# Performance work log

Hardware: AMD Instinct MI355X
Metric: run time of the kernel (lower is better)

## Reference

```python
import jax, jax.numpy as jnp
import numpy as np
import math

B, T, D = 2, 2048, 1024
NH, DH = 16, 64
MLP = 4096


def setup_inputs() -> dict:
    key = jax.random.key(0)
    ks = jax.random.split(key, 10)
    xavier = lambda k, shape: jax.random.uniform(
        k, shape, jnp.float32,
        -math.sqrt(6.0 / (shape[0] + shape[1])), math.sqrt(6.0 / (shape[0] + shape[1])))
    return {
        "inputs": jax.random.normal(ks[0], (B, T, D), jnp.float32),
        "cond": jax.random.normal(ks[1], (B, D), jnp.float32),
        "attention_mask": jnp.zeros((T, T), jnp.bool_),
        # LayerNorm params
        "ln1_g": jnp.ones((D,), jnp.float32), "ln1_b": jnp.zeros((D,), jnp.float32),
        "ln2_g": jnp.ones((D,), jnp.float32), "ln2_b": jnp.zeros((D,), jnp.float32),
        # Attention params (torch Linear stores weight as [out,in]; we store [in,out])
        "w_qkv": xavier(ks[2], (D, 3 * D)),
        "w_out": xavier(ks[3], (D, D)),
        "b_out": jax.random.normal(ks[4], (D,), jnp.float32),
        # MLP params
        "w1": xavier(ks[5], (D, MLP)), "b1": jax.random.normal(ks[6], (MLP,), jnp.float32),
        "w2": xavier(ks[7], (MLP, D)), "b2": jax.random.normal(ks[8], (D,), jnp.float32),
    }


def layer_norm(x, g, b, eps=1e-5):
    mu = jnp.mean(x, axis=-1, keepdims=True)
    var = jnp.var(x, axis=-1, keepdims=True)
    return (x - mu) * jax.lax.rsqrt(var + eps) * g + b


def reference(inputs, cond, attention_mask, ln1_g, ln1_b, ln2_g, ln2_b,
              w_qkv, w_out, b_out, w1, b1, w2, b2):
    # del cond, attention_mask  (unused in use_rs_attn path)
    x = layer_norm(inputs, ln1_g, ln1_b)
    qkv = x @ w_qkv  # [B,T,3D]
    q, k, v = jnp.split(qkv, 3, axis=-1)
    # [B,T,D] -> [B,NH,T,DH]
    split_heads = lambda t: t.reshape(B, T, NH, DH).transpose(0, 2, 1, 3)
    q, k, v = split_heads(q), split_heads(k), split_heads(v)
    att = jnp.einsum('bhqd,bhkd->bhqk', q, k) * (1.0 / math.sqrt(DH))
    att = jax.nn.softmax(att, axis=-1)  # NOTE: no causal mask in original
    y = jnp.einsum('bhqk,bhkd->bhqd', att, v)
    y = y.transpose(0, 2, 1, 3).reshape(B, T, D)
    y = y @ w_out + b_out
    x = y + inputs  # residual (dropout = identity in eval)
    h = layer_norm(x, ln2_g, ln2_b)
    h = jax.nn.gelu(h @ w1 + b1, approximate=False)
    h = h @ w2 + b2
    return x + h
```

## Files before the change

kernel.cpp:

```cpp
#include <hip/hip_runtime.h>
#include <hip/hip_bf16.h>
#include <math.h>

using bf16 = __hip_bfloat16;
typedef __attribute__((ext_vector_type(8))) short bf16x8;
typedef __attribute__((ext_vector_type(4))) float f32x4;

#define B_   2
#define T_   2048
#define D_   1024
#define NH_  16
#define DH_  64
#define MLP_ 4096
#define ROWS (B_ * T_)
#define BHTD ((size_t)32 * 2048 * 64)
#define SCL 0.18033688011112042f

__device__ __forceinline__ void gload_lds16(const void* g, void* l) {
    __builtin_amdgcn_global_load_lds(
        (const __attribute__((address_space(1))) unsigned int*)g,
        (__attribute__((address_space(3))) unsigned int*)l, 16, 0, 0);
}

__device__ __forceinline__ unsigned pk_bf16(float a, float b) {
    unsigned lo = __bfloat16_as_ushort(__float2bfloat16(a));
    unsigned hi = __bfloat16_as_ushort(__float2bfloat16(b));
    return lo | (hi << 16);
}

__global__ void wtrans_kernel(const float* __restrict__ W, bf16* __restrict__ Wt,
                              int K, int N) {
    __shared__ float tile[32][33];
    int n0 = blockIdx.x * 32, k0 = blockIdx.y * 32;
    int tx = threadIdx.x, ty = threadIdx.y;
#pragma unroll
    for (int i = 0; i < 32; i += 8)
        tile[ty + i][tx] = W[(size_t)(k0 + ty + i) * N + n0 + tx];
    __syncthreads();
#pragma unroll
    for (int i = 0; i < 32; i += 8)
        Wt[(size_t)(n0 + ty + i) * K + k0 + tx] = __float2bfloat16(tile[tx][ty + i]);
}

__global__ void transpose_v_kernel(const bf16* __restrict__ V, bf16* __restrict__ Vt) {
    __shared__ bf16 tile[32][33];
    int bh = blockIdx.z;
    int t0 = blockIdx.x * 32;
    int d0 = blockIdx.y * 32;
    int tx = threadIdx.x, ty = threadIdx.y;
    const bf16* src = V + (size_t)bh * T_ * 64;
    bf16* dst = Vt + (size_t)bh * 64 * T_;
#pragma unroll
    for (int i = 0; i < 32; i += 8)
        tile[ty + i][tx] = src[(size_t)(t0 + ty + i) * 64 + d0 + tx];
    __syncthreads();
#pragma unroll
    for (int i = 0; i < 32; i += 8)
        dst[(size_t)(d0 + ty + i) * T_ + t0 + tx] = tile[tx][ty + i];
}

__global__ void ln_kernel(const float* __restrict__ x, const float* __restrict__ g,
                          const float* __restrict__ bta, bf16* __restrict__ out) {
    int row = blockIdx.x;
    int t = threadIdx.x;
    float4 v = ((const float4*)(x + (size_t)row * D_))[t];
    float s1 = v.x + v.y + v.z + v.w;
    float s2 = v.x * v.x + v.y * v.y + v.z * v.z + v.w * v.w;
#pragma unroll
    for (int m = 1; m < 64; m <<= 1) {
        s1 += __shfl_xor(s1, m);
        s2 += __shfl_xor(s2, m);
    }
    __shared__ float red[8];
    int wid = t >> 6, lane = t & 63;
    if (lane == 0) { red[wid] = s1; red[4 + wid] = s2; }
    __syncthreads();
    s1 = red[0] + red[1] + red[2] + red[3];
    s2 = red[4] + red[5] + red[6] + red[7];
    float mu = s1 * (1.0f / D_);
    float var = s2 * (1.0f / D_) - mu * mu;
    float rs = rsqrtf(var + 1e-5f);
    float4 gv = ((const float4*)g)[t];
    float4 bv = ((const float4*)bta)[t];
    bf16* o = out + (size_t)row * D_ + t * 4;
    o[0] = __float2bfloat16((v.x - mu) * rs * gv.x + bv.x);
    o[1] = __float2bfloat16((v.y - mu) * rs * gv.y + bv.y);
    o[2] = __float2bfloat16((v.z - mu) * rs * gv.z + bv.z);
    o[3] = __float2bfloat16((v.w - mu) * rs * gv.w + bv.w);
}

template <int EPI, int BM>
__global__ __launch_bounds__(256) void gemm_bt(const bf16* __restrict__ A,
                                               const bf16* __restrict__ Bt,
                                               int N, int K,
                                               const float* __restrict__ bias,
                                               const float* __restrict__ resid,
                                               void* __restrict__ out) {
    constexpr int MF = BM / 32;
    __shared__ __align__(16) bf16 Asm[BM * 64];
    __shared__ __align__(16) bf16 Bsm[128 * 64];
    int tid = threadIdx.x;
    int nwg = gridDim.x * gridDim.y;
    int wg = blockIdx.y * gridDim.x + blockIdx.x;
    int swz = (wg & 7) * (nwg >> 3) + (wg >> 3);
    int bm = (swz / gridDim.x) * BM;
    int bn = (swz % gridDim.x) * 128;
    int wid = tid >> 6, lane = tid & 63;
    int wr = wid >> 1, wc = wid & 1;
    f32x4 acc[MF][4];
#pragma unroll
    for (int m = 0; m < MF; m++)
#pragma unroll
        for (int n = 0; n < 4; n++) acc[m][n] = (f32x4){0.f, 0.f, 0.f, 0.f};

    for (int k0 = 0; k0 < K; k0 += 64) {
        __syncthreads();
#pragma unroll
        for (int i = 0; i < BM * 8 / 256; i++) {
            int c = tid + i * 256;
            int row = c >> 3;
            int sw = ((c & 7) ^ (row & 7)) * 8;
            gload_lds16(&A[(size_t)(bm + row) * K + k0 + sw], &Asm[c * 8]);
        }
#pragma unroll
        for (int i = 0; i < 4; i++) {
            int c = tid + i * 256;
            int row = c >> 3;
            int sw = ((c & 7) ^ (row & 7)) * 8;
            gload_lds16(&Bt[(size_t)(bn + row) * K + k0 + sw], &Bsm[c * 8]);
        }
        __syncthreads();
#pragma unroll
        for (int kk = 0; kk < 2; kk++) {
            int cc = kk * 4 + (lane >> 4);
            bf16x8 af[MF], bfr[4];
#pragma unroll
            for (int m = 0; m < MF; m++) {
                int ra = wr * (BM / 2) + m * 16 + (lane & 15);
                af[m] = *(const bf16x8*)&Asm[ra * 64 + ((cc ^ (ra & 7)) * 8)];
            }
#pragma unroll
            for (int n = 0; n < 4; n++) {
                int rb = wc * 64 + n * 16 + (lane & 15);
                bfr[n] = *(const bf16x8*)&Bsm[rb * 64 + ((cc ^ (rb & 7)) * 8)];
            }
#pragma unroll
            for (int m = 0; m < MF; m++)
#pragma unroll
                for (int n = 0; n < 4; n++)
                    acc[m][n] = __builtin_amdgcn_mfma_f32_16x16x32_bf16(af[m], bfr[n], acc[m][n], 0, 0, 0);
        }
    }
    int r0 = bm + wr * (BM / 2);
    int c0 = bn + wc * 64;
#pragma unroll
    for (int m = 0; m < MF; m++) {
#pragma unroll
        for (int n = 0; n < 4; n++) {
#pragma unroll
            for (int j = 0; j < 4; j++) {
                int r = r0 + m * 16 + (lane >> 4) * 4 + j;
                int c = c0 + n * 16 + (lane & 15);
                float v = acc[m][n][j];
                if constexpr (EPI == 0) {
                    int which = c >> 10, d = c & 1023;
                    int h = d >> 6, dh = d & 63;
                    int b = r >> 11, t = r & 2047;
                    if (which == 0) v *= SCL;
                    ((bf16*)out)[(((size_t)which * 32 + b * 16 + h) * 2048 + t) * 64 + dh] =
                        __float2bfloat16(v);
                } else if constexpr (EPI == 1) {
                    ((float*)out)[(size_t)r * N + c] = v + bias[c] + resid[(size_t)r * N + c];
                } else {
                    float u = v + bias[c];
                    float ge = 0.5f * u * (1.0f + erff(u * 0.70710678118f));
                    ((bf16*)out)[(size_t)r * N + c] = __float2bfloat16(ge);
                }
            }
        }
    }
}

__global__ __launch_bounds__(512) void attn_kernel(const bf16* __restrict__ Q,
                                                   const bf16* __restrict__ Kt,
                                                   const bf16* __restrict__ Vt,
                                                   bf16* __restrict__ Y) {
    __shared__ __align__(16) bf16 Ksm[64][72];
    __shared__ __align__(16) bf16 Vsm[64][72];
    __shared__ __align__(16) bf16 Psm[8][16][72];
    int tid = threadIdx.x;
    int wid = tid >> 6, lane = tid & 63;
    int bh = blockIdx.y;
    int q0 = blockIdx.x * 128 + wid * 16;
    const bf16* Qb = Q + (size_t)bh * T_ * 64;
    const bf16* Kb = Kt + (size_t)bh * T_ * 64;
    const bf16* Vb = Vt + (size_t)bh * 64 * T_;

    bf16x8 aq[2];
#pragma unroll
    for (int kk = 0; kk < 2; kk++)
        aq[kk] = *(const bf16x8*)&Qb[(size_t)(q0 + (lane & 15)) * 64 + kk * 32 + (lane >> 4) * 8];

    float mrow = -1e30f, lrow = 0.f;
    f32x4 o[4];
#pragma unroll
    for (int n = 0; n < 4; n++) o[n] = (f32x4){0.f, 0.f, 0.f, 0.f};

    for (int kt = 0; kt < T_ / 64; kt++) {
        __syncthreads();
        {
            int row = tid >> 3, col8 = (tid & 7) * 8;
            *(uint4*)&Ksm[row][col8] = *(const uint4*)&Kb[(size_t)(kt * 64 + row) * 64 + col8];
            *(uint4*)&Vsm[row][col8] = *(const uint4*)&Vb[(size_t)row * T_ + kt * 64 + col8];
        }
        __syncthreads();

        f32x4 s[4];
        __builtin_amdgcn_s_setprio(1);
#pragma unroll
        for (int n = 0; n < 4; n++) {
            bf16x8 k0f = *(const bf16x8*)&Ksm[n * 16 + (lane & 15)][(lane >> 4) * 8];
            bf16x8 k1f = *(const bf16x8*)&Ksm[n * 16 + (lane & 15)][32 + (lane >> 4) * 8];
            s[n] = __builtin_amdgcn_mfma_f32_16x16x32_bf16(k0f, aq[0], (f32x4){0.f, 0.f, 0.f, 0.f}, 0, 0, 0);
            s[n] = __builtin_amdgcn_mfma_f32_16x16x32_bf16(k1f, aq[1], s[n], 0, 0, 0);
        }
        __builtin_amdgcn_s_setprio(0);

        float my = fmaxf(fmaxf(fmaxf(s[0][0], s[0][1]), fmaxf(s[0][2], s[0][3])),
                         fmaxf(fmaxf(s[1][0], s[1][1]), fmaxf(s[1][2], s[1][3])));
        float my2 = fmaxf(fmaxf(fmaxf(s[2][0], s[2][1]), fmaxf(s[2][2], s[2][3])),
                          fmaxf(fmaxf(s[3][0], s[3][1]), fmaxf(s[3][2], s[3][3])));
        my = fmaxf(my, my2);
        my = fmaxf(my, __shfl_xor(my, 16));
        my = fmaxf(my, __shfl_xor(my, 32));

        if (__any(my - mrow > 8.0f)) {
            float mn = fmaxf(mrow, my);
            float sc = exp2f(mrow - mn);
            mrow = mn;
            lrow *= sc;
#pragma unroll
            for (int j = 0; j < 4; j++) {
                float scj = __shfl(sc, (lane >> 4) * 4 + j);
#pragma unroll
                for (int n = 0; n < 4; n++) o[n][j] *= scj;
            }
        }

        float psum = 0.f;
#pragma unroll
        for (int n = 0; n < 4; n++)
#pragma unroll
            for (int j = 0; j < 4; j++) {
                float pv = exp2f(s[n][j] - mrow);
                s[n][j] = pv;
                psum += pv;
            }
        psum += __shfl_xor(psum, 16);
        psum += __shfl_xor(psum, 32);
        lrow += psum;

#pragma unroll
        for (int n = 0; n < 4; n++) {
            uint2 w;
            w.x = pk_bf16(s[n][0], s[n][1]);
            w.y = pk_bf16(s[n][2], s[n][3]);
            *(uint2*)&Psm[wid][lane & 15][n * 16 + (lane >> 4) * 4] = w;
        }

        bf16x8 pa[2];
#pragma unroll
        for (int kk = 0; kk < 2; kk++)
            pa[kk] = *(const bf16x8*)&Psm[wid][lane & 15][kk * 32 + (lane >> 4) * 8];

        __builtin_amdgcn_s_setprio(1);
#pragma unroll
        for (int n = 0; n < 4; n++) {
            bf16x8 v0 = *(const bf16x8*)&Vsm[n * 16 + (lane & 15)][(lane >> 4) * 8];
            bf16x8 v1 = *(const bf16x8*)&Vsm[n * 16 + (lane & 15)][32 + (lane >> 4) * 8];
            o[n] = __builtin_amdgcn_mfma_f32_16x16x32_bf16(pa[0], v0, o[n], 0, 0, 0);
            o[n] = __builtin_amdgcn_mfma_f32_16x16x32_bf16(pa[1], v1, o[n], 0, 0, 0);
        }
        __builtin_amdgcn_s_setprio(0);
    }

    int b = bh >> 4, h = bh & 15;
#pragma unroll
    for (int j = 0; j < 4; j++) {
        float lj = __shfl(lrow, (lane >> 4) * 4 + j);
        float inv = 1.0f / lj;
        int t = q0 + (lane >> 4) * 4 + j;
#pragma unroll
        for (int n = 0; n < 4; n++) {
            int c = h * 64 + n * 16 + (lane & 15);
            Y[((size_t)b * T_ + t) * D_ + c] = __float2bfloat16(o[n][j] * inv);
        }
    }
}

extern "C" void kernel_launch(void* const* d_in, const int* in_sizes, int n_in,
                              void* d_out, int out_size, void* d_ws, size_t ws_size,
                              hipStream_t stream) {
    const float* inputs = (const float*)d_in[0];
    const float* ln1_g = (const float*)d_in[3];
    const float* ln1_b = (const float*)d_in[4];
    const float* ln2_g = (const float*)d_in[5];
    const float* ln2_b = (const float*)d_in[6];
    const float* w_qkv = (const float*)d_in[7];
    const float* w_out = (const float*)d_in[8];
    const float* b_out = (const float*)d_in[9];
    const float* w1    = (const float*)d_in[10];
    const float* b1    = (const float*)d_in[11];
    const float* w2    = (const float*)d_in[12];
    const float* b2    = (const float*)d_in[13];

    char* p = (char*)d_ws;
    auto alloc = [&](size_t bytes) {
        void* r = (void*)p;
        p += (bytes + 255) & ~(size_t)255;
        return r;
    };
    bf16* x1     = (bf16*)alloc((size_t)ROWS * D_ * 2);
    bf16* wqkv_t = (bf16*)alloc((size_t)3 * D_ * D_ * 2);
    bf16* wout_t = (bf16*)alloc((size_t)D_ * D_ * 2);
    bf16* w1_t   = (bf16*)alloc((size_t)MLP_ * D_ * 2);
    bf16* w2_t   = (bf16*)alloc((size_t)D_ * MLP_ * 2);
    bf16* qkv    = (bf16*)alloc((size_t)3 * BHTD * 2);
    bf16* vt     = (bf16*)alloc((size_t)BHTD * 2);
    bf16* y      = (bf16*)alloc((size_t)ROWS * D_ * 2);
    float* x2    = (float*)alloc((size_t)ROWS * D_ * 4);
    bf16* h2     = (bf16*)alloc((size_t)ROWS * D_ * 2);
    bf16* act    = (bf16*)alloc((size_t)ROWS * MLP_ * 2);

    dim3 tb(32, 8);
    wtrans_kernel<<<dim3(3 * D_ / 32, D_ / 32), tb, 0, stream>>>(w_qkv, wqkv_t, D_, 3 * D_);
    wtrans_kernel<<<dim3(D_ / 32, D_ / 32), tb, 0, stream>>>(w_out, wout_t, D_, D_);
    wtrans_kernel<<<dim3(MLP_ / 32, D_ / 32), tb, 0, stream>>>(w1, w1_t, D_, MLP_);
    wtrans_kernel<<<dim3(D_ / 32, MLP_ / 32), tb, 0, stream>>>(w2, w2_t, MLP_, D_);

    ln_kernel<<<ROWS, 256, 0, stream>>>(inputs, ln1_g, ln1_b, x1);

    gemm_bt<0, 128><<<dim3(3 * D_ / 128, ROWS / 128), 256, 0, stream>>>(
        x1, wqkv_t, 3 * D_, D_, nullptr, nullptr, (void*)qkv);

    transpose_v_kernel<<<dim3(T_ / 32, 2, 32), tb, 0, stream>>>(qkv + 2 * BHTD, vt);

    attn_kernel<<<dim3(T_ / 128, 32), 512, 0, stream>>>(qkv, qkv + BHTD, vt, y);

    gemm_bt<1, 64><<<dim3(D_ / 128, ROWS / 64), 256, 0, stream>>>(
        y, wout_t, D_, D_, b_out, inputs, (void*)x2);

    ln_kernel<<<ROWS, 256, 0, stream>>>(x2, ln2_g, ln2_b, h2);

    gemm_bt<2, 128><<<dim3(MLP_ / 128, ROWS / 128), 256, 0, stream>>>(
        h2, w1_t, MLP_, D_, b1, nullptr, (void*)act);

    gemm_bt<1, 64><<<dim3(D_ / 128, ROWS / 64), 256, 0, stream>>>(
        act, w2_t, D_, MLP_, b2, x2, d_out);
}
```

Before: 425.5 us.

## Double-buffer GEMM LDS tiles and prefetch attention K/V into registers

The GEMM now keeps two LDS buffers and issues the async global-to-LDS loads for the next K slice before computing on the current one, with a single barrier per iteration. The attention kernel preloads the next K/V tile into registers while the current tile is processed. Both aim to hide global memory latency behind MFMA work. The cost is twice the GEMM shared memory and extra registers in attention, which may lower occupancy.

New measurement: 393.6 us. 1.08x faster.

```diff
diff --git a/kernel.cpp b/kernel.cpp
--- a/kernel.cpp
+++ b/kernel.cpp
@@ -97,8 +97,8 @@
                                                const float* __restrict__ resid,
                                                void* __restrict__ out) {
     constexpr int MF = BM / 32;
-    __shared__ __align__(16) bf16 Asm[BM * 64];
-    __shared__ __align__(16) bf16 Bsm[128 * 64];
+    __shared__ __align__(16) bf16 Asm[2][BM * 64];
+    __shared__ __align__(16) bf16 Bsm[2][128 * 64];
     int tid = threadIdx.x;
     int nwg = gridDim.x * gridDim.y;
     int wg = blockIdx.y * gridDim.x + blockIdx.x;
@@ -113,23 +113,29 @@
 #pragma unroll
         for (int n = 0; n < 4; n++) acc[m][n] = (f32x4){0.f, 0.f, 0.f, 0.f};
 
-    for (int k0 = 0; k0 < K; k0 += 64) {
-        __syncthreads();
+    auto stage = [&](int buf, int k0) {
 #pragma unroll
         for (int i = 0; i < BM * 8 / 256; i++) {
             int c = tid + i * 256;
             int row = c >> 3;
             int sw = ((c & 7) ^ (row & 7)) * 8;
-            gload_lds16(&A[(size_t)(bm + row) * K + k0 + sw], &Asm[c * 8]);
+            gload_lds16(&A[(size_t)(bm + row) * K + k0 + sw], &Asm[buf][c * 8]);
         }
 #pragma unroll
         for (int i = 0; i < 4; i++) {
             int c = tid + i * 256;
             int row = c >> 3;
             int sw = ((c & 7) ^ (row & 7)) * 8;
-            gload_lds16(&Bt[(size_t)(bn + row) * K + k0 + sw], &Bsm[c * 8]);
-        }
-        __syncthreads();
+            gload_lds16(&Bt[(size_t)(bn + row) * K + k0 + sw], &Bsm[buf][c * 8]);
+        }
+    };
+
+    stage(0, 0);
+    __syncthreads();
+    int NS = K / 64;
+    for (int s = 0; s < NS; s++) {
+        int cur = s & 1;
+        if (s + 1 < NS) stage(cur ^ 1, (s + 1) * 64);
 #pragma unroll
         for (int kk = 0; kk < 2; kk++) {
             int cc = kk * 4 + (lane >> 4);
@@ -137,12 +143,12 @@
 #pragma unroll
             for (int m = 0; m < MF; m++) {
                 int ra = wr * (BM / 2) + m * 16 + (lane & 15);
-                af[m] = *(const bf16x8*)&Asm[ra * 64 + ((cc ^ (ra & 7)) * 8)];
+                af[m] = *(const bf16x8*)&Asm[cur][ra * 64 + ((cc ^ (ra & 7)) * 8)];
             }
 #pragma unroll
             for (int n = 0; n < 4; n++) {
                 int rb = wc * 64 + n * 16 + (lane & 15);
-                bfr[n] = *(const bf16x8*)&Bsm[rb * 64 + ((cc ^ (rb & 7)) * 8)];
+                bfr[n] = *(const bf16x8*)&Bsm[cur][rb * 64 + ((cc ^ (rb & 7)) * 8)];
             }
 #pragma unroll
             for (int m = 0; m < MF; m++)
@@ -150,6 +156,7 @@
                 for (int n = 0; n < 4; n++)
                     acc[m][n] = __builtin_amdgcn_mfma_f32_16x16x32_bf16(af[m], bfr[n], acc[m][n], 0, 0, 0);
         }
+        __syncthreads();
     }
     int r0 = bm + wr * (BM / 2);
     int c0 = bn + wc * 64;
@@ -206,12 +213,17 @@
 #pragma unroll
     for (int n = 0; n < 4; n++) o[n] = (f32x4){0.f, 0.f, 0.f, 0.f};
 
+    int srow = tid >> 3, scol8 = (tid & 7) * 8;
+    uint4 kreg = *(const uint4*)&Kb[(size_t)srow * 64 + scol8];
+    uint4 vreg = *(const uint4*)&Vb[(size_t)srow * T_ + scol8];
+
     for (int kt = 0; kt < T_ / 64; kt++) {
         __syncthreads();
-        {
-            int row = tid >> 3, col8 = (tid & 7) * 8;
-            *(uint4*)&Ksm[row][col8] = *(const uint4*)&Kb[(size_t)(kt * 64 + row) * 64 + col8];
-            *(uint4*)&Vsm[row][col8] = *(const uint4*)&Vb[(size_t)row * T_ + kt * 64 + col8];
+        *(uint4*)&Ksm[srow][scol8] = kreg;
+        *(uint4*)&Vsm[srow][scol8] = vreg;
+        if (kt + 1 < T_ / 64) {
+            kreg = *(const uint4*)&Kb[(size_t)((kt + 1) * 64 + srow) * 64 + scol8];
+            vreg = *(const uint4*)&Vb[(size_t)srow * T_ + (kt + 1) * 64 + scol8];
         }
         __syncthreads();
 
```
